# Performance work log

Hardware: AMD Instinct MI355X
Metric: run time of the kernel (lower is better)

## Reference

```python
import jax, jax.numpy as jnp
import numpy as np

N, F, P, E, HID = 50000, 4, 12, 1_600_000, 64  # nodes, input feats, periods (FH), edges, hidden


def setup_inputs() -> dict:
    key = jax.random.key(0)
    ks = jax.random.split(key, 16)

    def nrm(k, shp, scale=0.1):
        return jax.random.normal(k, shp, jnp.float32) * scale

    inp = {
        "x": jax.random.normal(ks[0], (N, F, P), jnp.float32),
        "edge_index": jax.random.randint(ks[1], (2, E), 0, N),
        "edge_weights": jax.random.uniform(ks[2], (E,), jnp.float32),
        "att": nrm(ks[3], (P,), 1.0),
    }
    i = 4
    for g in ("z", "r", "h"):  # TGCN gate params: GCNConv weight/bias + Linear(2*hid, hid)
        inp[f"Wg_{g}"] = nrm(ks[i], (F, HID))
        inp[f"bg_{g}"] = jnp.zeros((HID,), jnp.float32)
        inp[f"Wl_{g}"] = nrm(jax.random.fold_in(ks[i], 1), (2 * HID, HID))
        inp[f"bl_{g}"] = jnp.zeros((HID,), jnp.float32)
        i += 1
    for j in range(1, 5):
        inp[f"W{j}"] = nrm(ks[i], (HID, HID))
        inp[f"b{j}"] = jnp.zeros((HID,), jnp.float32)
        i += 1
    inp["Wo"] = nrm(ks[i], (HID, P * F))
    inp["bo"] = jnp.zeros((P * F,), jnp.float32)
    return inp


def _gcn_norm(edge_index, ew):
    # GCNConv default: add self loops (weight 1), symmetric D^-1/2 (A+I) D^-1/2 normalization
    src, dst = edge_index[0], edge_index[1]
    loop = jnp.arange(N)
    src_f = jnp.concatenate([src, loop])
    dst_f = jnp.concatenate([dst, loop])
    ew_f = jnp.concatenate([ew, jnp.ones((N,), ew.dtype)])
    deg = jax.ops.segment_sum(ew_f, dst_f, num_segments=N)
    dinv = jnp.where(deg > 0, jax.lax.rsqrt(deg), 0.0)
    norm = dinv[src_f] * ew_f * dinv[dst_f]
    return src_f, dst_f, norm


def _gcn(x, W, b, src, dst, norm):
    xw = x @ W                               # [N, HID] transform before propagate
    msg = xw[src] * norm[:, None]            # gather + scale, [E+N, HID]
    return jax.ops.segment_sum(msg, dst, num_segments=N) + b


def reference(x, edge_index, edge_weights, att,
              Wg_z, bg_z, Wl_z, bl_z,
              Wg_r, bg_r, Wl_r, bl_r,
              Wg_h, bg_h, Wl_h, bl_h,
              W1, b1, W2, b2, W3, b3, W4, b4, Wo, bo):
    src, dst, norm = _gcn_norm(edge_index, edge_weights)

    def tgcn_cell(xt):
        # A3TGCN passes H=None every period -> H starts at zeros each period
        Hz = jnp.zeros((xt.shape[0], HID), xt.dtype)
        z = jax.nn.sigmoid(jnp.concatenate([_gcn(xt, Wg_z, bg_z, src, dst, norm), Hz], -1) @ Wl_z + bl_z)
        r = jax.nn.sigmoid(jnp.concatenate([_gcn(xt, Wg_r, bg_r, src, dst, norm), Hz], -1) @ Wl_r + bl_r)
        htil = jnp.tanh(jnp.concatenate([_gcn(xt, Wg_h, bg_h, src, dst, norm), Hz * r], -1) @ Wl_h + bl_h)
        return z * Hz + (1.0 - z) * htil

    probs = jax.nn.softmax(att)
    h = jnp.zeros((N, HID), x.dtype)
    for p in range(P):  # small fixed period loop keeps peak memory at one period's messages
        h = h + probs[p] * tgcn_cell(x[:, :, p])

    h = jax.nn.relu(h)
    h = h @ W1 + b1
    h = h @ W2 + b2
    h = h @ W3 + b3
    h = h @ W4 + b4
    h = h @ Wo + bo                          # [N, FH*F]
    return h.reshape(-1, F, P)
```

## Files before the change

kernel.cpp:

```cpp
#include <hip/hip_runtime.h>
#include <hip/hip_fp16.h>

#define FP 48
#define HID 64
#define NP 12
#define PL 65
#define NBB 256
#define BT 1024
#define CAPB 4864

__device__ __forceinline__ void mm_stage(const float* __restrict__ Alds,
                                         const float* __restrict__ Wg,
                                         float* __restrict__ Clds, int t)
{
    const int rg = (t >> 4) * 4, cg = (t & 15) * 4;
    float acc[4][4] = {};
    for (int k = 0; k < 64; ++k) {
        float a0 = Alds[(rg + 0) * PL + k];
        float a1 = Alds[(rg + 1) * PL + k];
        float a2 = Alds[(rg + 2) * PL + k];
        float a3 = Alds[(rg + 3) * PL + k];
        const float4 bv = *reinterpret_cast<const float4*>(Wg + k * 64 + cg);
        acc[0][0] += a0 * bv.x; acc[0][1] += a0 * bv.y; acc[0][2] += a0 * bv.z; acc[0][3] += a0 * bv.w;
        acc[1][0] += a1 * bv.x; acc[1][1] += a1 * bv.y; acc[1][2] += a1 * bv.z; acc[1][3] += a1 * bv.w;
        acc[2][0] += a2 * bv.x; acc[2][1] += a2 * bv.y; acc[2][2] += a2 * bv.z; acc[2][3] += a2 * bv.w;
        acc[3][0] += a3 * bv.x; acc[3][1] += a3 * bv.y; acc[3][2] += a3 * bv.z; acc[3][3] += a3 * bv.w;
    }
    for (int i = 0; i < 4; ++i)
        for (int j = 0; j < 4; ++j)
            Clds[(rg + i) * PL + cg + j] = acc[i][j];
}

__device__ __forceinline__ void bias_stage(const float* __restrict__ bin,
                                           const float* __restrict__ Wg,
                                           const float* __restrict__ badd,
                                           float* __restrict__ bout, int t)
{
    if (t < 64) {
        float s = badd[t];
        for (int k = 0; k < 64; ++k) s += bin[k] * Wg[k * 64 + t];
        bout[t] = s;
    }
}

__device__ void do_prep(
    const float* __restrict__ att,
    const float* __restrict__ Wg_z, const float* __restrict__ bg_z,
    const float* __restrict__ Wl_z, const float* __restrict__ bl_z,
    const float* __restrict__ Wg_h, const float* __restrict__ bg_h,
    const float* __restrict__ Wl_h, const float* __restrict__ bl_h,
    const float* __restrict__ W1, const float* __restrict__ b1,
    const float* __restrict__ W2, const float* __restrict__ b2,
    const float* __restrict__ W3, const float* __restrict__ b3,
    const float* __restrict__ W4, const float* __restrict__ b4,
    const float* __restrict__ Wo, const float* __restrict__ bo,
    float* __restrict__ probs, float* __restrict__ Mz, float* __restrict__ cz,
    float* __restrict__ Mh, float* __restrict__ ch,
    float* __restrict__ Wc, float* __restrict__ bc, int t)
{
    __shared__ float A[64 * PL];
    __shared__ float B[64 * PL];
    __shared__ float bias[64];
    __shared__ float bias2[64];

    if (t == 0) {
        float m = att[0];
        for (int p = 1; p < NP; ++p) m = fmaxf(m, att[p]);
        float e[NP]; float s = 0.f;
        for (int p = 0; p < NP; ++p) { e[p] = __expf(att[p] - m); s += e[p]; }
        float inv = 1.f / s;
        for (int p = 0; p < NP; ++p) probs[p] = e[p] * inv;
    }

    if (t < 256) {
        int f = t >> 6, j = t & 63;
        float az = 0.f, ah = 0.f;
        for (int k = 0; k < HID; ++k) {
            az += Wg_z[f * HID + k] * Wl_z[k * HID + j];
            ah += Wg_h[f * HID + k] * Wl_h[k * HID + j];
        }
        Mz[t] = az; Mh[t] = ah;
    }
    if (t < HID) {
        float az = bl_z[t], ah = bl_h[t];
        for (int k = 0; k < HID; ++k) {
            az += bg_z[k] * Wl_z[k * HID + t];
            ah += bg_h[k] * Wl_h[k * HID + t];
        }
        cz[t] = az; ch[t] = ah;
    }

    for (int idx = t; idx < 4096; idx += BT) {
        int i = idx >> 6, j = idx & 63;
        A[i * PL + j] = W1[idx];
    }
    if (t < 64) bias[t] = b1[t];
    __syncthreads();

    if (t < 256) mm_stage(A, W2, B, t);
    bias_stage(bias, W2, b2, bias2, t);
    __syncthreads();
    if (t < 256) mm_stage(B, W3, A, t);
    bias_stage(bias2, W3, b3, bias, t);
    __syncthreads();
    if (t < 256) mm_stage(A, W4, B, t);
    bias_stage(bias, W4, b4, bias2, t);
    __syncthreads();

    if (t < 256) {
        const int rg = (t >> 4) * 4, cg = (t & 15) * 4;
        if (cg < FP) {
            float acc[4][4] = {};
            for (int k = 0; k < 64; ++k) {
                float a0 = B[(rg + 0) * PL + k];
                float a1 = B[(rg + 1) * PL + k];
                float a2 = B[(rg + 2) * PL + k];
                float a3 = B[(rg + 3) * PL + k];
                const float4 bv = *reinterpret_cast<const float4*>(Wo + k * FP + cg);
                acc[0][0] += a0 * bv.x; acc[0][1] += a0 * bv.y; acc[0][2] += a0 * bv.z; acc[0][3] += a0 * bv.w;
                acc[1][0] += a1 * bv.x; acc[1][1] += a1 * bv.y; acc[1][2] += a1 * bv.z; acc[1][3] += a1 * bv.w;
                acc[2][0] += a2 * bv.x; acc[2][1] += a2 * bv.y; acc[2][2] += a2 * bv.z; acc[2][3] += a2 * bv.w;
                acc[3][0] += a3 * bv.x; acc[3][1] += a3 * bv.y; acc[3][2] += a3 * bv.z; acc[3][3] += a3 * bv.w;
            }
            for (int i = 0; i < 4; ++i)
                for (int j = 0; j < 4; ++j)
                    Wc[(rg + i) * FP + cg + j] = acc[i][j];
        }
        if (t < FP) {
            float s = bo[t];
            for (int k = 0; k < 64; ++k) s += bias2[k] * Wo[k * FP + t];
            bc[t] = s;
        }
    }
}

__global__ __launch_bounds__(BT) void build_kernel(
    const int* __restrict__ src, const int* __restrict__ dst,
    const float* __restrict__ ew,
    unsigned* __restrict__ cursor, int2* __restrict__ binned,
    int E, int CE, int NBUK,
    const float* __restrict__ att,
    const float* __restrict__ Wg_z, const float* __restrict__ bg_z,
    const float* __restrict__ Wl_z, const float* __restrict__ bl_z,
    const float* __restrict__ Wg_h, const float* __restrict__ bg_h,
    const float* __restrict__ Wl_h, const float* __restrict__ bl_h,
    const float* __restrict__ W1, const float* __restrict__ b1,
    const float* __restrict__ W2, const float* __restrict__ b2,
    const float* __restrict__ W3, const float* __restrict__ b3,
    const float* __restrict__ W4, const float* __restrict__ b4,
    const float* __restrict__ Wo, const float* __restrict__ bo,
    float* __restrict__ probs, float* __restrict__ Mz, float* __restrict__ cz,
    float* __restrict__ Mh, float* __restrict__ ch,
    float* __restrict__ Wc, float* __restrict__ bc)
{
    const int t = threadIdx.x;
    if (blockIdx.x == NBB) {
        do_prep(att, Wg_z, bg_z, Wl_z, bl_z, Wg_h, bg_h, Wl_h, bl_h,
                W1, b1, W2, b2, W3, b3, W4, b4, Wo, bo,
                probs, Mz, cz, Mh, ch, Wc, bc, t);
        return;
    }
    __shared__ int cnt[512];
    __shared__ int off[512];
    const int base = blockIdx.x * CE;
    for (int i = t; i < NBUK; i += BT) cnt[i] = 0;
    __syncthreads();

    for (int g = t; 4 * g < CE; g += BT) {
        const int e0 = base + 4 * g;
        if (e0 + 3 < E) {
            const int4 d4 = *reinterpret_cast<const int4*>(dst + e0);
            atomicAdd(&cnt[((unsigned)d4.x) >> 7], 1);
            atomicAdd(&cnt[((unsigned)d4.y) >> 7], 1);
            atomicAdd(&cnt[((unsigned)d4.z) >> 7], 1);
            atomicAdd(&cnt[((unsigned)d4.w) >> 7], 1);
        } else {
            for (int j = 0; j < 4; ++j)
                if (e0 + j < E)
                    atomicAdd(&cnt[((unsigned)dst[e0 + j]) >> 7], 1);
        }
    }
    __syncthreads();

    for (int i = t; i < NBUK; i += BT) {
        const int c = cnt[i];
        off[i] = c ? (int)atomicAdd(&cursor[i], (unsigned)c) : 0;
    }
    __syncthreads();

    for (int g = t; 4 * g < CE; g += BT) {
        const int e0 = base + 4 * g;
        if (e0 + 3 < E) {
            const int4   d4 = *reinterpret_cast<const int4*>(dst + e0);
            const int4   s4 = *reinterpret_cast<const int4*>(src + e0);
            const float4 w4 = *reinterpret_cast<const float4*>(ew + e0);
            {
                const int bk = ((unsigned)d4.x) >> 7;
                const int r = atomicAdd(&off[bk], 1);
                if (r < CAPB) binned[(size_t)bk * CAPB + r] =
                    make_int2(((d4.x & 127) << 16) | s4.x, __float_as_int(w4.x));
            }
            {
                const int bk = ((unsigned)d4.y) >> 7;
                const int r = atomicAdd(&off[bk], 1);
                if (r < CAPB) binned[(size_t)bk * CAPB + r] =
                    make_int2(((d4.y & 127) << 16) | s4.y, __float_as_int(w4.y));
            }
            {
                const int bk = ((unsigned)d4.z) >> 7;
                const int r = atomicAdd(&off[bk], 1);
                if (r < CAPB) binned[(size_t)bk * CAPB + r] =
                    make_int2(((d4.z & 127) << 16) | s4.z, __float_as_int(w4.z));
            }
            {
                const int bk = ((unsigned)d4.w) >> 7;
                const int r = atomicAdd(&off[bk], 1);
                if (r < CAPB) binned[(size_t)bk * CAPB + r] =
                    make_int2(((d4.w & 127) << 16) | s4.w, __float_as_int(w4.w));
            }
        } else {
            for (int j = 0; j < 4; ++j) {
                const int e = e0 + j;
                if (e < E) {
                    const int d = dst[e];
                    const int bk = ((unsigned)d) >> 7;
                    const int r = atomicAdd(&off[bk], 1);
                    if (r < CAPB) binned[(size_t)bk * CAPB + r] =
                        make_int2(((d & 127) << 16) | src[e], __float_as_int(ew[e]));
                }
            }
        }
    }
}

__global__ __launch_bounds__(512) void csr_convert_kernel(
    const int2* __restrict__ binned, const unsigned* __restrict__ cursor,
    unsigned* __restrict__ csr, int2* __restrict__ nodeinfo,
    const float* __restrict__ x,
    unsigned short* __restrict__ xs, int N, int NBUK)
{
    const int t = threadIdx.x;
    const int b = blockIdx.x;
    const int node0 = b << 7;
    const int nend = min(128, N - node0);
    const int ebeg = b * CAPB;
    const int ecnt = min((int)cursor[b], CAPB);

    __shared__ int   cnt[128];
    __shared__ float fsum[128];
    __shared__ int   pfx[128];
    __shared__ float sdi[128];

    if (t < 128) { cnt[t] = 0; fsum[t] = 0.f; }
    __syncthreads();

    int4 ev4[5];
    #pragma unroll
    for (int i = 0; i < 5; ++i) {
        const int o = i * 1024 + 2 * t;
        int4 v = make_int4(-1, 0, -1, 0);
        if (o < ecnt) {
            v = *reinterpret_cast<const int4*>(binned + ebeg + o);
            if (o + 1 >= ecnt) v.z = -1;
        }
        ev4[i] = v;
    }

    #pragma unroll
    for (int i = 0; i < 5; ++i) {
        if (ev4[i].x >= 0) {
            const int dl = (ev4[i].x >> 16) & 127;
            atomicAdd(&cnt[dl], 1);
            atomicAdd(&fsum[dl], __int_as_float(ev4[i].y));
        }
        if (ev4[i].z >= 0) {
            const int dl = (ev4[i].z >> 16) & 127;
            atomicAdd(&cnt[dl], 1);
            atomicAdd(&fsum[dl], __int_as_float(ev4[i].w));
        }
    }
    __syncthreads();

    const int myc = (t < 128) ? cnt[t] : 0;
    if (t < 128) pfx[t] = myc;
    __syncthreads();
    for (int off = 1; off < 128; off <<= 1) {
        int tmp = 0;
        if (t < 128 && t >= off) tmp = pfx[t - off];
        __syncthreads();
        if (t < 128 && t >= off) pfx[t] += tmp;
        __syncthreads();
    }

    if (t < 128) {
        const int excl = pfx[t] - myc;
        const float di = rsqrtf(1.f + fsum[t]);
        sdi[t] = di;
        if (t < nend)
            nodeinfo[node0 + t] = make_int2((myc << 22) | (ebeg + excl), __float_as_int(di));
        cnt[t] = ebeg + excl;
    }
    __syncthreads();

    #pragma unroll
    for (int i = 0; i < 5; ++i) {
        if (ev4[i].x >= 0) {
            const int dl = (ev4[i].x >> 16) & 127;
            const int pos = atomicAdd(&cnt[dl], 1);
            const float w = __int_as_float(ev4[i].y);
            const unsigned hb = (unsigned)__half_as_ushort(__float2half_rn(w));
            csr[pos] = (unsigned)(ev4[i].x & 0xffff) | (hb << 16);
        }
        if (ev4[i].z >= 0) {
            const int dl = (ev4[i].z >> 16) & 127;
            const int pos = atomicAdd(&cnt[dl], 1);
            const float w = __int_as_float(ev4[i].w);
            const unsigned hb = (unsigned)__half_as_ushort(__float2half_rn(w));
            csr[pos] = (unsigned)(ev4[i].z & 0xffff) | (hb << 16);
        }
    }

    const int gtot = nend * 6;
    for (int g = t; g < gtot; g += 512) {
        const int nl = g / 6;
        const int q = g - nl * 6;
        const float dsc = sdi[nl];
        const float* xr = x + (size_t)(node0 + nl) * FP + q * 8;
        const float4 v0 = *reinterpret_cast<const float4*>(xr);
        const float4 v1 = *reinterpret_cast<const float4*>(xr + 4);
        unsigned p0 = (unsigned)__half_as_ushort(__float2half_rn(dsc * v0.x)) |
                      ((unsigned)__half_as_ushort(__float2half_rn(dsc * v0.y)) << 16);
        unsigned p1 = (unsigned)__half_as_ushort(__float2half_rn(dsc * v0.z)) |
                      ((unsigned)__half_as_ushort(__float2half_rn(dsc * v0.w)) << 16);
        unsigned p2 = (unsigned)__half_as_ushort(__float2half_rn(dsc * v1.x)) |
                      ((unsigned)__half_as_ushort(__float2half_rn(dsc * v1.y)) << 16);
        unsigned p3 = (unsigned)__half_as_ushort(__float2half_rn(dsc * v1.z)) |
                      ((unsigned)__half_as_ushort(__float2half_rn(dsc * v1.w)) << 16);
        *reinterpret_cast<int4*>(xs + (size_t)(node0 + nl) * FP + q * 8) =
            make_int4((int)p0, (int)p1, (int)p2, (int)p3);
    }
}

__global__ __launch_bounds__(256) void gather_node_kernel(
    const unsigned short* __restrict__ xs, const float* __restrict__ x,
    const int2* __restrict__ nodeinfo,
    const unsigned* __restrict__ csr,
    const float* __restrict__ probs,
    const float* __restrict__ Mz, const float* __restrict__ cz,
    const float* __restrict__ Mh, const float* __restrict__ ch,
    const float* __restrict__ Wc, const float* __restrict__ bc,
    float* __restrict__ out, int N)
{
    __shared__ __align__(16) float sWc[HID * FP];
    __shared__ __align__(16) float sprobs[16];
    __shared__ __align__(16) float yacc[4][384];
    __shared__ __align__(16) float yld[4][FP];
    __shared__ __align__(16) float hld[4][HID];
    for (int i = threadIdx.x; i < HID * FP; i += 256) sWc[i] = Wc[i];
    if (threadIdx.x < NP) sprobs[threadIdx.x] = probs[threadIdx.x];
    __syncthreads();

    const int lane = threadIdx.x & 63;
    const int wib  = threadIdx.x >> 6;
    const int n    = blockIdx.x * 4 + wib;
    if (n >= N) return;

    const int slot = lane >> 3;
    const int q    = lane & 7;
    const bool act = (q < 6);
    const int qc   = act ? q : 5;
    const char* xsb = (const char*)xs;

    const int2 ni = nodeinfo[n];
    const int beg = ni.x & 0x3FFFFF;
    const int end = beg + (int)((unsigned)ni.x >> 22);
    const float di = __int_as_float(ni.y);

    float a0 = 0.f, a1 = 0.f, a2 = 0.f, a3 = 0.f;
    float a4 = 0.f, a5 = 0.f, a6 = 0.f, a7 = 0.f;
    #pragma unroll 2
    for (int e = beg + slot; e < end; e += 8) {
        const unsigned ev = csr[e];
        const float w = __half2float(__ushort_as_half((unsigned short)(ev >> 16)));
        const unsigned soff = (ev & 0xffffu) * 96u;
        const int4 xv = *reinterpret_cast<const int4*>(xsb + soff + (qc << 4));
        const float2 f0 = __half22float2(*reinterpret_cast<const __half2*>(&xv.x));
        const float2 f1 = __half22float2(*reinterpret_cast<const __half2*>(&xv.y));
        const float2 f2 = __half22float2(*reinterpret_cast<const __half2*>(&xv.z));
        const float2 f3 = __half22float2(*reinterpret_cast<const __half2*>(&xv.w));
        a0 = fmaf(w, f0.x, a0); a1 = fmaf(w, f0.y, a1);
        a2 = fmaf(w, f1.x, a2); a3 = fmaf(w, f1.y, a3);
        a4 = fmaf(w, f2.x, a4); a5 = fmaf(w, f2.y, a5);
        a6 = fmaf(w, f3.x, a6); a7 = fmaf(w, f3.y, a7);
    }

    if (act) {
        float* dst0 = &yacc[wib][slot * 48 + q * 8];
        *reinterpret_cast<float4*>(dst0)     = make_float4(a0, a1, a2, a3);
        *reinterpret_cast<float4*>(dst0 + 4) = make_float4(a4, a5, a6, a7);
    }

    if (lane < FP) {
        const float* yf = yacc[wib];
        float s = 0.f;
        #pragma unroll
        for (int sl = 0; sl < 8; ++sl) s += yf[sl * 48 + lane];
        float xself = x[(size_t)n * FP + lane];
        float yv = di * s + di * di * xself;
        int f = lane / 12;
        int p = lane - f * 12;
        yld[wib][p * 4 + f] = yv;
    }

    const float mz0 = Mz[lane], mz1 = Mz[64 + lane], mz2 = Mz[128 + lane], mz3 = Mz[192 + lane];
    const float mh0 = Mh[lane], mh1 = Mh[64 + lane], mh2 = Mh[128 + lane], mh3 = Mh[192 + lane];
    const float czv = cz[lane], chv = ch[lane];
    const int   c   = (lane < FP) ? lane : 0;
    const float bcv = bc[c];

    const float* yw = yld[wib];
    float hacc = 0.f;
    #pragma unroll
    for (int p = 0; p < NP; ++p) {
        const float4 v = *reinterpret_cast<const float4*>(yw + p * 4);
        float az = czv + v.x * mz0 + v.y * mz1 + v.z * mz2 + v.w * mz3;
        float ah = chv + v.x * mh0 + v.y * mh1 + v.z * mh2 + v.w * mh3;
        float g  = __builtin_amdgcn_rcpf(1.f + __expf(az));
        float ahc = fminf(fmaxf(ah, -15.f), 15.f);
        float eh = __expf(2.f * ahc);
        float th = 1.f - 2.f * __builtin_amdgcn_rcpf(eh + 1.f);
        hacc += sprobs[p] * g * th;
    }
    hacc = fmaxf(hacc, 0.f);

    hld[wib][lane] = hacc;
    const float* hw = hld[wib];
    float o = bcv;
    #pragma unroll
    for (int i4 = 0; i4 < 16; ++i4) {
        const float4 h4 = *reinterpret_cast<const float4*>(hw + i4 * 4);
        o += h4.x * sWc[(i4 * 4 + 0) * FP + c];
        o += h4.y * sWc[(i4 * 4 + 1) * FP + c];
        o += h4.z * sWc[(i4 * 4 + 2) * FP + c];
        o += h4.w * sWc[(i4 * 4 + 3) * FP + c];
    }
    if (lane < FP) out[(size_t)n * FP + lane] = o;
}

extern "C" void kernel_launch(void* const* d_in, const int* in_sizes, int n_in,
                              void* d_out, int out_size, void* d_ws, size_t ws_size,
                              hipStream_t stream)
{
    const int N = in_sizes[0] / FP;
    const int E = in_sizes[1] / 2;
    const int NBUK = (N + 127) >> 7;
    const int CE = (((E + NBB - 1) / NBB) + 3) & ~3;

    const float* x    = (const float*)d_in[0];
    const int*   ei   = (const int*)d_in[1];
    const float* ew   = (const float*)d_in[2];
    const float* att  = (const float*)d_in[3];
    const float* Wg_z = (const float*)d_in[4];
    const float* bg_z = (const float*)d_in[5];
    const float* Wl_z = (const float*)d_in[6];
    const float* bl_z = (const float*)d_in[7];
    const float* Wg_h = (const float*)d_in[12];
    const float* bg_h = (const float*)d_in[13];
    const float* Wl_h = (const float*)d_in[14];
    const float* bl_h = (const float*)d_in[15];
    const float* W1 = (const float*)d_in[16]; const float* b1 = (const float*)d_in[17];
    const float* W2 = (const float*)d_in[18]; const float* b2 = (const float*)d_in[19];
    const float* W3 = (const float*)d_in[20]; const float* b3 = (const float*)d_in[21];
    const float* W4 = (const float*)d_in[22]; const float* b4 = (const float*)d_in[23];
    const float* Wo = (const float*)d_in[24]; const float* bo = (const float*)d_in[25];

    const int* srcp = ei;
    const int* dstp = ei + E;

    int2* binned       = (int2*)d_ws;
    unsigned* csr      = (unsigned*)(binned + (size_t)NBUK * CAPB + 8);
    unsigned short* xs = (unsigned short*)(csr + (size_t)NBUK * CAPB);
    unsigned* cursor   = (unsigned*)(xs + (size_t)N * FP);
    int2* nodeinfo     = (int2*)(cursor + 512);
    float* probs       = (float*)(nodeinfo + N);
    float* Mz          = probs + 16;
    float* cz          = Mz + 256;
    float* Mh          = cz + 64;
    float* ch          = Mh + 256;
    float* Wc          = ch + 64;
    float* bc          = Wc + HID * FP;

    hipMemsetAsync(cursor, 0, (size_t)NBUK * sizeof(unsigned), stream);

    build_kernel<<<NBB + 1, BT, 0, stream>>>(
        srcp, dstp, ew, cursor, binned, E, CE, NBUK,
        att, Wg_z, bg_z, Wl_z, bl_z, Wg_h, bg_h, Wl_h, bl_h,
        W1, b1, W2, b2, W3, b3, W4, b4, Wo, bo,
        probs, Mz, cz, Mh, ch, Wc, bc);

    csr_convert_kernel<<<NBUK, 512, 0, stream>>>(binned, cursor, csr, nodeinfo,
                                                 x, xs, N, NBUK);

    gather_node_kernel<<<(N + 3) / 4, 256, 0, stream>>>(xs, x, nodeinfo, csr,
                                                        probs, Mz, cz, Mh, ch, Wc, bc,
                                                        (float*)d_out, N);
}
```

Measured before the change: 255.9 us.

## Fuse edge binning and CSR conversion into one kernel with grid barrier

Merges the bucket-binning kernel and the CSR conversion kernel into a single launch. An atomic counter acts as a software grid barrier, and the 256 binning blocks then loop over the buckets to do the conversion. Shared memory becomes one aliased buffer so the prep, binning and conversion phases can reuse it. This removes one kernel launch and its gap, but it relies on all 257 blocks being co-resident for the spin barrier. The conversion now runs on 256 blocks, each handling about two buckets in sequence, with int2 loads instead of int4.

```diff
diff --git a/kernel.cpp b/kernel.cpp
--- a/kernel.cpp
+++ b/kernel.cpp
@@ -56,12 +56,13 @@
     const float* __restrict__ Wo, const float* __restrict__ bo,
     float* __restrict__ probs, float* __restrict__ Mz, float* __restrict__ cz,
     float* __restrict__ Mh, float* __restrict__ ch,
-    float* __restrict__ Wc, float* __restrict__ bc, int t)
+    float* __restrict__ Wc, float* __restrict__ bc,
+    float* __restrict__ smem, int t)
 {
-    __shared__ float A[64 * PL];
-    __shared__ float B[64 * PL];
-    __shared__ float bias[64];
-    __shared__ float bias2[64];
+    float* A     = smem;
+    float* B     = smem + 4160;
+    float* bias  = smem + 8320;
+    float* bias2 = smem + 8384;
 
     if (t == 0) {
         float m = att[0];
@@ -134,11 +135,14 @@
     }
 }
 
-__global__ __launch_bounds__(BT) void build_kernel(
+__global__ __launch_bounds__(BT, 8) void build_csr_kernel(
     const int* __restrict__ src, const int* __restrict__ dst,
     const float* __restrict__ ew,
-    unsigned* __restrict__ cursor, int2* __restrict__ binned,
-    int E, int CE, int NBUK,
+    unsigned* __restrict__ cursor, unsigned* __restrict__ done,
+    int2* __restrict__ binned, unsigned* __restrict__ csr,
+    int2* __restrict__ nodeinfo, const float* __restrict__ x,
+    unsigned short* __restrict__ xs,
+    int E, int CE, int NBUK, int N,
     const float* __restrict__ att,
     const float* __restrict__ Wg_z, const float* __restrict__ bg_z,
     const float* __restrict__ Wl_z, const float* __restrict__ bl_z,
@@ -153,191 +157,186 @@
     float* __restrict__ Mh, float* __restrict__ ch,
     float* __restrict__ Wc, float* __restrict__ bc)
 {
+    __shared__ __align__(16) float smem[8448];
     const int t = threadIdx.x;
-    if (blockIdx.x == NBB) {
+    const int bid = blockIdx.x;
+
+    if (bid == NBB) {
         do_prep(att, Wg_z, bg_z, Wl_z, bl_z, Wg_h, bg_h, Wl_h, bl_h,
                 W1, b1, W2, b2, W3, b3, W4, b4, Wo, bo,
-                probs, Mz, cz, Mh, ch, Wc, bc, t);
+                probs, Mz, cz, Mh, ch, Wc, bc, smem, t);
         return;
     }
-    __shared__ int cnt[512];
-    __shared__ int off[512];
-    const int base = blockIdx.x * CE;
-    for (int i = t; i < NBUK; i += BT) cnt[i] = 0;
-    __syncthreads();
-
-    for (int g = t; 4 * g < CE; g += BT) {
-        const int e0 = base + 4 * g;
-        if (e0 + 3 < E) {
-            const int4 d4 = *reinterpret_cast<const int4*>(dst + e0);
-            atomicAdd(&cnt[((unsigned)d4.x) >> 7], 1);
-            atomicAdd(&cnt[((unsigned)d4.y) >> 7], 1);
-            atomicAdd(&cnt[((unsigned)d4.z) >> 7], 1);
-            atomicAdd(&cnt[((unsigned)d4.w) >> 7], 1);
-        } else {
-            for (int j = 0; j < 4; ++j)
-                if (e0 + j < E)
-                    atomicAdd(&cnt[((unsigned)dst[e0 + j]) >> 7], 1);
-        }
-    }
-    __syncthreads();
-
-    for (int i = t; i < NBUK; i += BT) {
-        const int c = cnt[i];
-        off[i] = c ? (int)atomicAdd(&cursor[i], (unsigned)c) : 0;
-    }
-    __syncthreads();
-
-    for (int g = t; 4 * g < CE; g += BT) {
-        const int e0 = base + 4 * g;
-        if (e0 + 3 < E) {
-            const int4   d4 = *reinterpret_cast<const int4*>(dst + e0);
-            const int4   s4 = *reinterpret_cast<const int4*>(src + e0);
-            const float4 w4 = *reinterpret_cast<const float4*>(ew + e0);
-            {
-                const int bk = ((unsigned)d4.x) >> 7;
-                const int r = atomicAdd(&off[bk], 1);
-                if (r < CAPB) binned[(size_t)bk * CAPB + r] =
-                    make_int2(((d4.x & 127) << 16) | s4.x, __float_as_int(w4.x));
-            }
-            {
-                const int bk = ((unsigned)d4.y) >> 7;
-                const int r = atomicAdd(&off[bk], 1);
-                if (r < CAPB) binned[(size_t)bk * CAPB + r] =
-                    make_int2(((d4.y & 127) << 16) | s4.y, __float_as_int(w4.y));
-            }
-            {
-                const int bk = ((unsigned)d4.z) >> 7;
-                const int r = atomicAdd(&off[bk], 1);
-                if (r < CAPB) binned[(size_t)bk * CAPB + r] =
-                    make_int2(((d4.z & 127) << 16) | s4.z, __float_as_int(w4.z));
-            }
-            {
-                const int bk = ((unsigned)d4.w) >> 7;
-                const int r = atomicAdd(&off[bk], 1);
-                if (r < CAPB) binned[(size_t)bk * CAPB + r] =
-                    make_int2(((d4.w & 127) << 16) | s4.w, __float_as_int(w4.w));
-            }
-        } else {
-            for (int j = 0; j < 4; ++j) {
-                const int e = e0 + j;
-                if (e < E) {
-                    const int d = dst[e];
-                    const int bk = ((unsigned)d) >> 7;
+
+    {
+        int* cnt = (int*)smem;
+        int* off = (int*)smem + 512;
+        const int base = bid * CE;
+        for (int i = t; i < NBUK; i += BT) cnt[i] = 0;
+        __syncthreads();
+
+        for (int g = t; 4 * g < CE; g += BT) {
+            const int e0 = base + 4 * g;
+            if (e0 + 3 < E) {
+                const int4 d4 = *reinterpret_cast<const int4*>(dst + e0);
+                atomicAdd(&cnt[((unsigned)d4.x) >> 7], 1);
+                atomicAdd(&cnt[((unsigned)d4.y) >> 7], 1);
+                atomicAdd(&cnt[((unsigned)d4.z) >> 7], 1);
+                atomicAdd(&cnt[((unsigned)d4.w) >> 7], 1);
+            } else {
+                for (int j = 0; j < 4; ++j)
+                    if (e0 + j < E)
+                        atomicAdd(&cnt[((unsigned)dst[e0 + j]) >> 7], 1);
+            }
+        }
+        __syncthreads();
+
+        for (int i = t; i < NBUK; i += BT) {
+            const int c = cnt[i];
+            off[i] = c ? (int)atomicAdd(&cursor[i], (unsigned)c) : 0;
+        }
+        __syncthreads();
+
+        for (int g = t; 4 * g < CE; g += BT) {
+            const int e0 = base + 4 * g;
+            if (e0 + 3 < E) {
+                const int4   d4 = *reinterpret_cast<const int4*>(dst + e0);
+                const int4   s4 = *reinterpret_cast<const int4*>(src + e0);
+                const float4 w4 = *reinterpret_cast<const float4*>(ew + e0);
+                {
+                    const int bk = ((unsigned)d4.x) >> 7;
                     const int r = atomicAdd(&off[bk], 1);
                     if (r < CAPB) binned[(size_t)bk * CAPB + r] =
-                        make_int2(((d & 127) << 16) | src[e], __float_as_int(ew[e]));
-                }
-            }
-        }
-    }
-}
-
-__global__ __launch_bounds__(512) void csr_convert_kernel(
-    const int2* __restrict__ binned, const unsigned* __restrict__ cursor,
-    unsigned* __restrict__ csr, int2* __restrict__ nodeinfo,
-    const float* __restrict__ x,
-    unsigned short* __restrict__ xs, int N, int NBUK)
-{
-    const int t = threadIdx.x;
-    const int b = blockIdx.x;
-    const int node0 = b << 7;
-    const int nend = min(128, N - node0);
-    const int ebeg = b * CAPB;
-    const int ecnt = min((int)cursor[b], CAPB);
-
-    __shared__ int   cnt[128];
-    __shared__ float fsum[128];
-    __shared__ int   pfx[128];
-    __shared__ float sdi[128];
-
-    if (t < 128) { cnt[t] = 0; fsum[t] = 0.f; }
-    __syncthreads();
-
-    int4 ev4[5];
-    #pragma unroll
-    for (int i = 0; i < 5; ++i) {
-        const int o = i * 1024 + 2 * t;
-        int4 v = make_int4(-1, 0, -1, 0);
-        if (o < ecnt) {
-            v = *reinterpret_cast<const int4*>(binned + ebeg + o);
-            if (o + 1 >= ecnt) v.z = -1;
-        }
-        ev4[i] = v;
-    }
-
-    #pragma unroll
-    for (int i = 0; i < 5; ++i) {
-        if (ev4[i].x >= 0) {
-            const int dl = (ev4[i].x >> 16) & 127;
-            atomicAdd(&cnt[dl], 1);
-            atomicAdd(&fsum[dl], __int_as_float(ev4[i].y));
-        }
-        if (ev4[i].z >= 0) {
-            const int dl = (ev4[i].z >> 16) & 127;
-            atomicAdd(&cnt[dl], 1);
-            atomicAdd(&fsum[dl], __int_as_float(ev4[i].w));
-        }
-    }
-    __syncthreads();
-
-    const int myc = (t < 128) ? cnt[t] : 0;
-    if (t < 128) pfx[t] = myc;
-    __syncthreads();
-    for (int off = 1; off < 128; off <<= 1) {
-        int tmp = 0;
-        if (t < 128 && t >= off) tmp = pfx[t - off];
-        __syncthreads();
-        if (t < 128 && t >= off) pfx[t] += tmp;
-        __syncthreads();
-    }
-
-    if (t < 128) {
-        const int excl = pfx[t] - myc;
-        const float di = rsqrtf(1.f + fsum[t]);
-        sdi[t] = di;
-        if (t < nend)
-            nodeinfo[node0 + t] = make_int2((myc << 22) | (ebeg + excl), __float_as_int(di));
-        cnt[t] = ebeg + excl;
-    }
-    __syncthreads();
-
-    #pragma unroll
-    for (int i = 0; i < 5; ++i) {
-        if (ev4[i].x >= 0) {
-            const int dl = (ev4[i].x >> 16) & 127;
-            const int pos = atomicAdd(&cnt[dl], 1);
-            const float w = __int_as_float(ev4[i].y);
-            const unsigned hb = (unsigned)__half_as_ushort(__float2half_rn(w));
-            csr[pos] = (unsigned)(ev4[i].x & 0xffff) | (hb << 16);
-        }
-        if (ev4[i].z >= 0) {
-            const int dl = (ev4[i].z >> 16) & 127;
-            const int pos = atomicAdd(&cnt[dl], 1);
-            const float w = __int_as_float(ev4[i].w);
-            const unsigned hb = (unsigned)__half_as_ushort(__float2half_rn(w));
-            csr[pos] = (unsigned)(ev4[i].z & 0xffff) | (hb << 16);
-        }
-    }
-
-    const int gtot = nend * 6;
-    for (int g = t; g < gtot; g += 512) {
-        const int nl = g / 6;
-        const int q = g - nl * 6;
-        const float dsc = sdi[nl];
-        const float* xr = x + (size_t)(node0 + nl) * FP + q * 8;
-        const float4 v0 = *reinterpret_cast<const float4*>(xr);
-        const float4 v1 = *reinterpret_cast<const float4*>(xr + 4);
-        unsigned p0 = (unsigned)__half_as_ushort(__float2half_rn(dsc * v0.x)) |
-                      ((unsigned)__half_as_ushort(__float2half_rn(dsc * v0.y)) << 16);
-        unsigned p1 = (unsigned)__half_as_ushort(__float2half_rn(dsc * v0.z)) |
-                      ((unsigned)__half_as_ushort(__float2half_rn(dsc * v0.w)) << 16);
-        unsigned p2 = (unsigned)__half_as_ushort(__float2half_rn(dsc * v1.x)) |
-                      ((unsigned)__half_as_ushort(__float2half_rn(dsc * v1.y)) << 16);
-        unsigned p3 = (unsigned)__half_as_ushort(__float2half_rn(dsc * v1.z)) |
-                      ((unsigned)__half_as_ushort(__float2half_rn(dsc * v1.w)) << 16);
-        *reinterpret_cast<int4*>(xs + (size_t)(node0 + nl) * FP + q * 8) =
-            make_int4((int)p0, (int)p1, (int)p2, (int)p3);
+                        make_int2(((d4.x & 127) << 16) | s4.x, __float_as_int(w4.x));
+                }
+                {
+                    const int bk = ((unsigned)d4.y) >> 7;
+                    const int r = atomicAdd(&off[bk], 1);
+                    if (r < CAPB) binned[(size_t)bk * CAPB + r] =
+                        make_int2(((d4.y & 127) << 16) | s4.y, __float_as_int(w4.y));
+                }
+                {
+                    const int bk = ((unsigned)d4.z) >> 7;
+                    const int r = atomicAdd(&off[bk], 1);
+                    if (r < CAPB) binned[(size_t)bk * CAPB + r] =
+                        make_int2(((d4.z & 127) << 16) | s4.z, __float_as_int(w4.z));
+                }
+                {
+                    const int bk = ((unsigned)d4.w) >> 7;
+                    const int r = atomicAdd(&off[bk], 1);
+                    if (r < CAPB) binned[(size_t)bk * CAPB + r] =
+                        make_int2(((d4.w & 127) << 16) | s4.w, __float_as_int(w4.w));
+                }
+            } else {
+                for (int j = 0; j < 4; ++j) {
+                    const int e = e0 + j;
+                    if (e < E) {
+                        const int d = dst[e];
+                        const int bk = ((unsigned)d) >> 7;
+                        const int r = atomicAdd(&off[bk], 1);
+                        if (r < CAPB) binned[(size_t)bk * CAPB + r] =
+                            make_int2(((d & 127) << 16) | src[e], __float_as_int(ew[e]));
+                    }
+                }
+            }
+        }
+    }
+
+    __syncthreads();
+    __threadfence();
+    if (t == 0) {
+        atomicAdd(done, 1u);
+        while (atomicAdd(done, 0u) < (unsigned)NBB)
+            __builtin_amdgcn_s_sleep(2);
+    }
+    __syncthreads();
+    __threadfence();
+
+    {
+        int*   ccnt  = (int*)smem;
+        float* cfsum = smem + 128;
+        int*   cpfx  = (int*)smem + 256;
+        float* csdi  = smem + 384;
+
+        for (int b = bid; b < NBUK; b += NBB) {
+            const int node0 = b << 7;
+            const int nend = min(128, N - node0);
+            const int ebeg = b * CAPB;
+            const int ecnt = min((int)cursor[b], CAPB);
+
+            if (t < 128) { ccnt[t] = 0; cfsum[t] = 0.f; }
+            __syncthreads();
+
+            int2 ev[5];
+            #pragma unroll
+            for (int i = 0; i < 5; ++i) {
+                const int o = i * BT + t;
+                ev[i] = (o < ecnt) ? binned[ebeg + o] : make_int2(-1, 0);
+            }
+            #pragma unroll
+            for (int i = 0; i < 5; ++i) {
+                if (ev[i].x >= 0) {
+                    const int dl = (ev[i].x >> 16) & 127;
+                    atomicAdd(&ccnt[dl], 1);
+                    atomicAdd(&cfsum[dl], __int_as_float(ev[i].y));
+                }
+            }
+            __syncthreads();
+
+            const int myc = (t < 128) ? ccnt[t] : 0;
+            if (t < 128) cpfx[t] = myc;
+            __syncthreads();
+            for (int off = 1; off < 128; off <<= 1) {
+                int tmp = 0;
+                if (t < 128 && t >= off) tmp = cpfx[t - off];
+                __syncthreads();
+                if (t < 128 && t >= off) cpfx[t] += tmp;
+                __syncthreads();
+            }
+
+            if (t < 128) {
+                const int excl = cpfx[t] - myc;
+                const float di = rsqrtf(1.f + cfsum[t]);
+                csdi[t] = di;
+                if (t < nend)
+                    nodeinfo[node0 + t] =
+                        make_int2((myc << 22) | (ebeg + excl), __float_as_int(di));
+                ccnt[t] = ebeg + excl;
+            }
+            __syncthreads();
+
+            #pragma unroll
+            for (int i = 0; i < 5; ++i) {
+                if (ev[i].x >= 0) {
+                    const int dl = (ev[i].x >> 16) & 127;
+                    const int pos = atomicAdd(&ccnt[dl], 1);
+                    const float w = __int_as_float(ev[i].y);
+                    const unsigned hb = (unsigned)__half_as_ushort(__float2half_rn(w));
+                    csr[pos] = (unsigned)(ev[i].x & 0xffff) | (hb << 16);
+                }
+            }
+
+            const int gtot = nend * 6;
+            for (int g = t; g < gtot; g += BT) {
+                const int nl = g / 6;
+                const int q = g - nl * 6;
+                const float dsc = csdi[nl];
+                const float* xr = x + (size_t)(node0 + nl) * FP + q * 8;
+                const float4 v0 = *reinterpret_cast<const float4*>(xr);
+                const float4 v1 = *reinterpret_cast<const float4*>(xr + 4);
+                unsigned p0 = (unsigned)__half_as_ushort(__float2half_rn(dsc * v0.x)) |
+                              ((unsigned)__half_as_ushort(__float2half_rn(dsc * v0.y)) << 16);
+                unsigned p1 = (unsigned)__half_as_ushort(__float2half_rn(dsc * v0.z)) |
+                              ((unsigned)__half_as_ushort(__float2half_rn(dsc * v0.w)) << 16);
+                unsigned p2 = (unsigned)__half_as_ushort(__float2half_rn(dsc * v1.x)) |
+                              ((unsigned)__half_as_ushort(__float2half_rn(dsc * v1.y)) << 16);
+                unsigned p3 = (unsigned)__half_as_ushort(__float2half_rn(dsc * v1.z)) |
+                              ((unsigned)__half_as_ushort(__float2half_rn(dsc * v1.w)) << 16);
+                *reinterpret_cast<int4*>(xs + (size_t)(node0 + nl) * FP + q * 8) =
+                    make_int4((int)p0, (int)p1, (int)p2, (int)p3);
+            }
+            __syncthreads();
+        }
     }
 }
 
@@ -481,6 +480,7 @@
     unsigned* csr      = (unsigned*)(binned + (size_t)NBUK * CAPB + 8);
     unsigned short* xs = (unsigned short*)(csr + (size_t)NBUK * CAPB);
     unsigned* cursor   = (unsigned*)(xs + (size_t)N * FP);
+    unsigned* done     = cursor + 500;
     int2* nodeinfo     = (int2*)(cursor + 512);
     float* probs       = (float*)(nodeinfo + N);
     float* Mz          = probs + 16;
@@ -490,16 +490,14 @@
     float* Wc          = ch + 64;
     float* bc          = Wc + HID * FP;
 
-    hipMemsetAsync(cursor, 0, (size_t)NBUK * sizeof(unsigned), stream);
-
-    build_kernel<<<NBB + 1, BT, 0, stream>>>(
-        srcp, dstp, ew, cursor, binned, E, CE, NBUK,
+    hipMemsetAsync(cursor, 0, 512 * sizeof(unsigned), stream);
+
+    build_csr_kernel<<<NBB + 1, BT, 0, stream>>>(
+        srcp, dstp, ew, cursor, done, binned, csr, nodeinfo, x, xs,
+        E, CE, NBUK, N,
         att, Wg_z, bg_z, Wl_z, bl_z, Wg_h, bg_h, Wl_h, bl_h,
         W1, b1, W2, b2, W3, b3, W4, b4, Wo, bo,
         probs, Mz, cz, Mh, ch, Wc, bc);
-
-    csr_convert_kernel<<<NBUK, 512, 0, stream>>>(binned, cursor, csr, nodeinfo,
-                                                 x, xs, N, NBUK);
 
     gather_node_kernel<<<(N + 3) / 4, 256, 0, stream>>>(xs, x, nodeinfo, csr,
                                                         probs, Mz, cz, Mh, ch, Wc, bc,
```

Result: slower. 413.6 us (+61.6%).
